# Optimization experiments

Hardware: AMD Instinct MI355X
Metric: run time of the kernel (lower is better)

## Reference

```python
import jax, jax.numpy as jnp
import numpy as np
from jax import lax

B, L, R = 128, 256, 36
D_TXT, D_IMG, D_SOC = 768, 2048, 10
EPS = 0.05 ** 2        # geomloss blur=0.05, p=2 -> epsilon = blur^p
N_ITERS = 20           # fixed log-domain Sinkhorn iterations
GAMMA = 0.01


def _pcost(x, y):
    # x: [B,n,d], y: [B,m,d] -> C_ij = ||x_i - y_j||^2 / 2 (geomloss p=2 cost)
    xx = jnp.sum(x * x, -1)[:, :, None]
    yy = jnp.sum(y * y, -1)[:, None, :]
    xy = jnp.einsum('bnd,bmd->bnm', x, y)
    return 0.5 * (xx + yy - 2.0 * xy)


def _sinkhorn_cost(C, loga, logb, eps, n_iters):
    # Log-domain Sinkhorn; masked points carry loga/logb = -inf (zero weight).
    f = jnp.zeros(loga.shape, C.dtype)
    g = jnp.zeros(logb.shape, C.dtype)

    def body(fg, _):
        f, g = fg
        g = -eps * jax.nn.logsumexp(loga[:, :, None] + (f[:, :, None] - C) / eps, axis=1)
        f = -eps * jax.nn.logsumexp(logb[:, None, :] + (g[:, None, :] - C) / eps, axis=2)
        return (f, g), None

    (f, g), _ = lax.scan(body, (f, g), None, length=n_iters)
    a = jnp.exp(loga)  # exp(-inf) = 0 for masked entries
    b = jnp.exp(logb)
    return jnp.sum(a * f, -1) + jnp.sum(b * g, -1)  # <a,f> + <b,g>


def _forward(txt_global, txt_region, img_global, img_region, social, attn_mask,
             W_stat, b_stat, W_gt, b_gt, W_gi, b_gi, W_rt, b_rt, W_ri, b_ri,
             W_m1, b_m1, W_m2, b_m2):
    relu = jax.nn.relu
    soc = relu(social @ W_stat + b_stat)                            # [B,100]
    tg = relu(jnp.concatenate([txt_global, soc], axis=1) @ W_gt + b_gt)  # [B,200]
    ig = relu(img_global @ W_gi + b_gi)                              # [B,200]
    h = relu((tg + ig) @ W_m1 + b_m1)
    mix_pred = h @ W_m2 + b_m2                                       # [B,2]

    tr = relu(txt_region @ W_rt + b_rt)                              # [B,L,50]
    ir = relu(img_region @ W_ri + b_ri)                              # [B,R,50]

    Bn, _, _ = tr.shape
    Rn = ir.shape[1]
    mask = attn_mask > 0
    n_words = jnp.sum(attn_mask, axis=-1).astype(tr.dtype)          # [B]
    loga = jnp.where(mask, -jnp.log(n_words)[:, None], -jnp.inf)    # uniform over valid tokens
    logb = jnp.full((Bn, Rn), -jnp.log(float(Rn)), tr.dtype)        # uniform over regions

    # Debiased Sinkhorn divergence (geomloss SamplesLoss default debias=True):
    Sxy = _sinkhorn_cost(_pcost(tr, ir), loga, logb, EPS, N_ITERS)
    Sxx = _sinkhorn_cost(_pcost(tr, tr), loga, loga, EPS, N_ITERS)
    Syy = _sinkhorn_cost(_pcost(ir, ir), logb, logb, EPS, N_ITERS)
    w_dis = Sxy - 0.5 * (Sxx + Syy)                                  # [B]

    w_pred = jnp.stack([1.0 - GAMMA * w_dis, GAMMA * w_dis], axis=1)  # [B,2]
    logit = jax.nn.softmax(jnp.maximum(mix_pred, w_pred), axis=1)
    return logit


def setup_inputs() -> dict:
    key = jax.random.key(0)
    ks = jax.random.split(key, 24)
    init = lambda k, s: (jax.random.normal(k, s) * 0.02).astype(jnp.float32)
    lengths = jax.random.randint(ks[0], (B,), 16, L + 1)             # ragged lengths
    attn_mask = (jnp.arange(L)[None, :] < lengths[:, None]).astype(jnp.int32)
    return {
        'txt_global': jax.random.normal(ks[1], (B, D_TXT), jnp.float32),
        'txt_region': jax.random.normal(ks[2], (B, L, D_TXT), jnp.float32),
        'img_global': jax.random.normal(ks[3], (B, D_IMG), jnp.float32),
        'img_region': jax.random.normal(ks[4], (B, R, D_IMG), jnp.float32),
        'social': jax.random.normal(ks[5], (B, D_SOC), jnp.float32),
        'attn_mask': attn_mask,
        'W_stat': init(ks[6], (D_SOC, 100)), 'b_stat': jnp.zeros((100,), jnp.float32),
        'W_gt': init(ks[7], (868, 200)), 'b_gt': jnp.zeros((200,), jnp.float32),
        'W_gi': init(ks[8], (D_IMG, 200)), 'b_gi': jnp.zeros((200,), jnp.float32),
        'W_rt': init(ks[9], (D_TXT, 50)), 'b_rt': jnp.zeros((50,), jnp.float32),
        'W_ri': init(ks[10], (D_IMG, 50)), 'b_ri': jnp.zeros((50,), jnp.float32),
        'W_m1': init(ks[11], (200, 100)), 'b_m1': jnp.zeros((100,), jnp.float32),
        'W_m2': init(ks[12], (100, 2)), 'b_m2': jnp.zeros((2,), jnp.float32),
    }


def reference(txt_global, txt_region, img_global, img_region, social, attn_mask,
              W_stat, b_stat, W_gt, b_gt, W_gi, b_gi, W_rt, b_rt, W_ri, b_ri,
              W_m1, b_m1, W_m2, b_m2):
    return _forward(txt_global, txt_region, img_global, img_region, social, attn_mask,
                    W_stat, b_stat, W_gt, b_gt, W_gi, b_gi, W_rt, b_rt, W_ri, b_ri,
                    W_m1, b_m1, W_m2, b_m2)
```

## Files before the change

### kernel.cpp

```cpp
#include <hip/hip_runtime.h>

typedef float        f32x4 __attribute__((ext_vector_type(4)));
typedef short        s16x8 __attribute__((ext_vector_type(8)));
typedef unsigned int u32x4 __attribute__((ext_vector_type(4)));

#define EPS_LN2      0.0017328679513998632f
#define INV_EPS_LN2  577.0780163555852f
#define LOG2_36      5.169925001442312f

__device__ __forceinline__ short f2bf(float x) {
  unsigned int u; __builtin_memcpy(&u, &x, 4);
  u = (u + 0x7FFFu + ((u >> 16) & 1u)) >> 16;
  return (short)u;
}

__device__ __forceinline__ unsigned short f2h(float x) {
  return __builtin_bit_cast(unsigned short, (_Float16)x);
}
__device__ __forceinline__ float h2f(unsigned short h) {
  return (float)__builtin_bit_cast(_Float16, h);
}

#define GLOAD16(g, l) __builtin_amdgcn_global_load_lds( \
    (const __attribute__((address_space(1))) void*)(g), \
    (__attribute__((address_space(3))) void*)(l), 16, 0, 0)

__global__ __launch_bounds__(256) void k_prep(
    const float* __restrict__ W_rt, const float* __restrict__ W_ri,
    short* __restrict__ frt, short* __restrict__ fri,
    const float* __restrict__ txt, const float* __restrict__ img,
    const float* __restrict__ social,
    const float* __restrict__ W_stat, const float* __restrict__ b_stat,
    const float* __restrict__ W_gt, const float* __restrict__ W_gi,
    float* __restrict__ pre) {
  __shared__ float sA[32][128];
  int bid = blockIdx.x;
  if (bid < 88) {
    int slot = bid * 256 + threadIdx.x;
    const float* W; short* dst; int f;
    if (slot < 6144) { W = W_rt; dst = frt; f = slot; }
    else             { W = W_ri; dst = fri; f = slot - 6144; }
    int k32 = f >> 8, rem = f & 255, ct = rem >> 6, l = rem & 63;
    int col = ct * 16 + (l & 15);
    int k0  = k32 * 32 + (l >> 4) * 8;
    s16x8 p;
#pragma unroll
    for (int c = 0; c < 8; ++c) {
      float v = (col < 50) ? W[(k0 + c) * 50 + col] : 0.f;
      p[c] = f2bf(v);
    }
    *(s16x8*)(dst + (long)f * 8) = p;
    return;
  }
  int gb = bid - 88;
  int job = gb >> 4, rb = (gb >> 2) & 3, cb = gb & 3;
  int t = threadIdx.x, r0 = rb * 32;
  const float* W; int k0, klen;
  if (job < 6)       { k0 = job * 128;       klen = 128; W = W_gt; }
  else if (job == 6) { k0 = 0;               klen = 100; W = W_gt + 768 * 200; }
  else               { k0 = (job - 7) * 128; klen = 128; W = W_gi; }
  if (job == 6) {
    for (int idx = t; idx < 4096; idx += 256) {
      int r = idx >> 7, k = idx & 127;
      float v = 0.f;
      if (k < 100) {
        v = b_stat[k];
#pragma unroll
        for (int u = 0; u < 10; ++u) v += social[(r0 + r) * 10 + u] * W_stat[u * 100 + k];
        v = fmaxf(v, 0.f);
      }
      sA[r][k] = v;
    }
  } else {
    const float* A = (job < 6) ? txt : img;
    int K_A = (job < 6) ? 768 : 2048;
    for (int idx = t; idx < 4096; idx += 256) {
      int r = idx >> 7, k = idx & 127;
      sA[r][k] = A[(r0 + r) * K_A + k0 + k];
    }
  }
  __syncthreads();
  int c = cb * 64 + (t & 63), rg = t >> 6;
  if (c < 200) {
    float acc[8];
#pragma unroll
    for (int i = 0; i < 8; ++i) acc[i] = 0.f;
    for (int k4 = 0; k4 < klen; k4 += 4) {
      float w0 = W[(k0 + k4    ) * 200 + c];
      float w1 = W[(k0 + k4 + 1) * 200 + c];
      float w2 = W[(k0 + k4 + 2) * 200 + c];
      float w3 = W[(k0 + k4 + 3) * 200 + c];
#pragma unroll
      for (int i = 0; i < 8; ++i) {
        f32x4 a = *(const f32x4*)&sA[rg * 8 + i][k4];
        acc[i] += a[0]*w0 + a[1]*w1 + a[2]*w2 + a[3]*w3;
      }
    }
    float* dst = pre + (long)job * 25600;
#pragma unroll
    for (int i = 0; i < 8; ++i)
      dst[(r0 + rg * 8 + i) * 200 + c] = acc[i];
  }
}

template<int K32>
__device__ __forceinline__ void proj_body(const float* __restrict__ A,
                                          const short* __restrict__ Bf,
                                          const float* __restrict__ bias,
                                          float* __restrict__ out, int bid,
                                          char* smem) {
  constexpr int KH = K32 / 2;
  int wave = threadIdx.x >> 6, lane = threadIdx.x & 63;
  int rg = wave >> 1, ks = wave & 1;
  int rl = lane & 15, q = lane >> 4, r7 = rl & 7;
  int row0 = bid * 32 + rg * 16;
  const int K = K32 * 32;
  char* wbuf = smem + wave * 18432;

  int ra = lane >> 3, pa = lane & 7;
  int fsw = (pa ^ ra) * 4;
  const float* asrc0 = A + (long)(row0 + ra)     * K + ks * (KH * 32) + fsw;
  const float* asrc1 = A + (long)(row0 + 8 + ra) * K + ks * (KH * 32) + fsw;
  const short* bsrc  = Bf + (long)ks * (KH * 2048) + lane * 8;

#define PSTAGE(KK, ST) { \
    char* ad = wbuf + (ST) * 6144; \
    GLOAD16(asrc0 + (KK) * 32, ad); \
    GLOAD16(asrc1 + (KK) * 32, ad + 1024); \
    char* bd = ad + 2048; \
    const short* bs = bsrc + (KK) * 2048; \
    GLOAD16(bs,        bd); \
    GLOAD16(bs + 512,  bd + 1024); \
    GLOAD16(bs + 1024, bd + 2048); \
    GLOAD16(bs + 1536, bd + 3072); \
  }

  f32x4 acc[4];
#pragma unroll
  for (int ct = 0; ct < 4; ++ct) acc[ct] = (f32x4){0.f, 0.f, 0.f, 0.f};

  PSTAGE(0, 0);
  PSTAGE(1, 1);
#pragma unroll
  for (int k = 0; k < KH; ++k) {
    if (k + 2 < KH) {
      PSTAGE(k + 2, (k + 2) % 3);
      asm volatile("s_waitcnt vmcnt(12)" ::: "memory");
    } else if (k + 2 == KH) {
      asm volatile("s_waitcnt vmcnt(6)" ::: "memory");
    } else {
      asm volatile("s_waitcnt vmcnt(0)" ::: "memory");
    }
    __builtin_amdgcn_sched_barrier(0);
    const char* ab = wbuf + (k % 3) * 6144;
    f32x4 a0 = *(const f32x4*)(ab + rl * 128 + (((q * 2)     ^ r7) << 4));
    f32x4 a1 = *(const f32x4*)(ab + rl * 128 + (((q * 2 + 1) ^ r7) << 4));
    const char* bb = ab + 2048;
    s16x8 af;
    af[0]=f2bf(a0[0]); af[1]=f2bf(a0[1]); af[2]=f2bf(a0[2]); af[3]=f2bf(a0[3]);
    af[4]=f2bf(a1[0]); af[5]=f2bf(a1[1]); af[6]=f2bf(a1[2]); af[7]=f2bf(a1[3]);
#pragma unroll
    for (int ct = 0; ct < 4; ++ct) {
      s16x8 bfr = *(const s16x8*)(bb + ct * 1024 + lane * 16);
      acc[ct] = __builtin_amdgcn_mfma_f32_16x16x32_bf16(af, bfr, acc[ct], 0, 0, 0);
    }
  }
#undef PSTAGE

  if (ks == 1) {
#pragma unroll
    for (int ct = 0; ct < 4; ++ct)
      *(f32x4*)(wbuf + ct * 1024 + lane * 16) = acc[ct];
  }
  __syncthreads();
  if (ks == 0) {
    const char* pb = smem + (wave + 1) * 18432;
#pragma unroll
    for (int ct = 0; ct < 4; ++ct) {
      f32x4 o = *(const f32x4*)(pb + ct * 1024 + lane * 16);
      int col = ct * 16 + rl;
      float bv = (col < 50) ? bias[col] : 0.f;
#pragma unroll
      for (int r = 0; r < 4; ++r) {
        int grow = row0 + q * 4 + r;
        float v = fmaxf(acc[ct][r] + o[r] + bv, 0.f);
        out[(long)grow * 64 + col] = (col < 50) ? v : 0.f;
      }
    }
  }
}

__device__ __forceinline__ void mix_body(
    int r, const float* __restrict__ pre,
    const float* __restrict__ b_gt, const float* __restrict__ b_gi,
    const float* __restrict__ W_m1, const float* __restrict__ b_m1,
    const float* __restrict__ W_m2, const float* __restrict__ b_m2,
    float* __restrict__ mix, float* smem) {
  float* sm = smem;
  float* sh = smem + 200;
  int t = threadIdx.x;
  if (t < 200) {
    float s1 = b_gt[t], s2 = b_gi[t];
#pragma unroll
    for (int j = 0; j < 7; ++j)  s1 += pre[(long)j * 25600 + r * 200 + t];
#pragma unroll
    for (int j = 7; j < 23; ++j) s2 += pre[(long)j * 25600 + r * 200 + t];
    sm[t] = fmaxf(s1, 0.f) + fmaxf(s2, 0.f);
  }
  __syncthreads();
  if (t < 100) {
    float a = b_m1[t];
#pragma unroll 4
    for (int k = 0; k < 200; ++k) a += sm[k] * W_m1[k * 100 + t];
    sh[t] = fmaxf(a, 0.f);
  }
  __syncthreads();
  if (t < 2) {
    float a = b_m2[t];
    for (int k = 0; k < 100; ++k) a += sh[k] * W_m2[k * 2 + t];
    mix[r * 2 + t] = a;
  }
}

__global__ __launch_bounds__(256)
void k_pm(
    const float* __restrict__ txt_region, const short* __restrict__ frt,
    const float* __restrict__ b_rt, float* __restrict__ tr,
    const float* __restrict__ img_region, const short* __restrict__ fri,
    const float* __restrict__ b_ri, float* __restrict__ ir,
    const float* __restrict__ pre,
    const float* __restrict__ b_gt, const float* __restrict__ b_gi,
    const float* __restrict__ W_m1, const float* __restrict__ b_m1,
    const float* __restrict__ W_m2, const float* __restrict__ b_m2,
    float* __restrict__ mix) {
  __shared__ __align__(16) char smem[73728];
  int bid = blockIdx.x;
  if (bid < 144)       proj_body<64>(img_region, fri, b_ri, ir, bid, smem);
  else if (bid < 1168) proj_body<24>(txt_region, frt, b_rt, tr, bid - 144, smem);
  else                 mix_body(bid - 1168, pre, b_gt, b_gi, W_m1, b_m1, W_m2, b_m2, mix, (float*)smem);
}

__global__ __launch_bounds__(256) void k_sxx(
    const float* __restrict__ tr, const int* __restrict__ amask,
    float* __restrict__ norms_g, float* __restrict__ Sxx) {
  __shared__ __align__(16) char smem[163840];
  char*  CT = smem;
  short* Xf = (short*)(smem + 131072);
  float*     sF   = (float*)(smem + 131072);
  float*     sG   = (float*)(smem + 132096);
  _Float16*  sA0  = (_Float16*)(smem + 133120);
  _Float16*  sA1  = (_Float16*)(smem + 133632);
  int b = blockIdx.x, tid = threadIdx.x;
  int lane = tid & 63, wv = tid >> 6;
  int q = lane >> 4, rl = lane & 15;

  int c = 0;
#pragma unroll
  for (int i = 0; i < 4; ++i) c += amask[b * 256 + i * 64 + lane];
#pragma unroll
  for (int o = 1; o < 64; o <<= 1) c += __shfl_xor(c, o);
  int n = __builtin_amdgcn_readfirstlane(c);

  const float* Xg = tr + (long)b * 256 * 64;
  for (int slot = tid; slot < 2048; slot += 256) {
    int t = slot >> 7, k32 = (slot >> 6) & 1, l = slot & 63;
    int row = t * 16 + (l & 15), k0 = k32 * 32 + (l >> 4) * 8;
    const float* src = Xg + row * 64 + k0;
    f32x4 a0 = *(const f32x4*)src, a1 = *(const f32x4*)(src + 4);
    s16x8 p;
    p[0]=f2bf(a0[0]); p[1]=f2bf(a0[1]); p[2]=f2bf(a0[2]); p[3]=f2bf(a0[3]);
    p[4]=f2bf(a1[0]); p[5]=f2bf(a1[1]); p[6]=f2bf(a1[2]); p[7]=f2bf(a1[3]);
    *(s16x8*)(Xf + slot * 8) = p;
  }
  __syncthreads();

  float* ng = norms_g + b * 256;
#pragma unroll
  for (int si = 0; si < 4; ++si) {
    int st = wv * 4 + si;
    s16x8 a0 = *(const s16x8*)(Xf + ((st * 2 + 0) * 64 + lane) * 8);
    s16x8 a1 = *(const s16x8*)(Xf + ((st * 2 + 1) * 64 + lane) * 8);
    f32x4 d = (f32x4){0.f, 0.f, 0.f, 0.f};
    d = __builtin_amdgcn_mfma_f32_16x16x32_bf16(a0, a0, d, 0, 0, 0);
    d = __builtin_amdgcn_mfma_f32_16x16x32_bf16(a1, a1, d, 0, 0, 0);
#pragma unroll
    for (int r = 0; r < 4; ++r)
      if (rl == q * 4 + r) ng[st * 16 + q * 4 + r] = d[r];
  }
  __syncthreads();

  float nj[16];
#pragma unroll
  for (int ct = 0; ct < 16; ++ct) nj[ct] = ng[ct * 16 + rl];

#pragma unroll
  for (int si = 0; si < 4; ++si) {
    int st = wv * 4 + si;
    int i0w = st * 16 + q * 4;
    float ni0 = ng[i0w], ni1 = ng[i0w + 1], ni2 = ng[i0w + 2], ni3 = ng[i0w + 3];
    s16x8 a0 = *(const s16x8*)(Xf + ((st * 2 + 0) * 64 + lane) * 8);
    s16x8 a1 = *(const s16x8*)(Xf + ((st * 2 + 1) * 64 + lane) * 8);
    f32x4 acc[16];
#pragma unroll
    for (int ct = 0; ct < 16; ++ct) acc[ct] = (f32x4){0.f, 0.f, 0.f, 0.f};
#pragma unroll
    for (int ct = 0; ct < 16; ++ct) {
      s16x8 b0 = *(const s16x8*)(Xf + ((ct * 2 + 0) * 64 + lane) * 8);
      s16x8 b1 = *(const s16x8*)(Xf + ((ct * 2 + 1) * 64 + lane) * 8);
      acc[ct] = __builtin_amdgcn_mfma_f32_16x16x32_bf16(a0, b0, acc[ct], 0, 0, 0);
      acc[ct] = __builtin_amdgcn_mfma_f32_16x16x32_bf16(a1, b1, acc[ct], 0, 0, 0);
    }
#pragma unroll
    for (int ct = 0; ct < 16; ++ct) {
      int j = ct * 16 + rl;
      float njv = nj[ct];
      float v0 = (acc[ct][0] - 0.5f * (ni0 + njv)) * INV_EPS_LN2;
      float v1 = (acc[ct][1] - 0.5f * (ni1 + njv)) * INV_EPS_LN2;
      float v2 = (acc[ct][2] - 0.5f * (ni2 + njv)) * INV_EPS_LN2;
      float v3 = (acc[ct][3] - 0.5f * (ni3 + njv)) * INV_EPS_LN2;
      char* p = CT + (((j << 9) + (i0w << 1)) ^ ((j & 7) << 4));
      *(unsigned*)(p)     = (unsigned)f2h(v0) | ((unsigned)f2h(v1) << 16);
      *(unsigned*)(p + 4) = (unsigned)f2h(v2) | ((unsigned)f2h(v3) << 16);
    }
  }
  __syncthreads();

  float log2n = log2f((float)n);
  sF[tid] = 0.f; sG[tid] = 0.f;
  sA0[tid] = (tid < n) ? (_Float16)(-log2n) : (_Float16)(-65504.f);
  sA1[tid] = (_Float16)(-65504.f);
  __syncthreads();

  int j = tid;
  unsigned base = (unsigned)(j << 9);
  unsigned sw   = (unsigned)((j & 7) << 4);
  int ns = (n + 7) >> 3;
  for (int h = 0; h < 40; ++h) {
    const unsigned* ah2 = (const unsigned*)((h & 1) ? sA1 : sA0);
    _Float16* aout = (h & 1) ? sA0 : sA1;
    if (j < n) {
      unsigned mm = 0xFBFFFBFFu;
      for (int s = 0; s < ns; ++s) {
        u32x4 v = *(const u32x4*)(CT + ((base + (unsigned)(s << 4)) ^ sw));
        unsigned a0 = ah2[s * 4 + 0], a1 = ah2[s * 4 + 1];
        unsigned a2 = ah2[s * 4 + 2], a3 = ah2[s * 4 + 3];
        unsigned t0, t1, t2, t3;
        asm("v_pk_add_f16 %0, %1, %2" : "=v"(t0) : "v"(v[0]), "v"(a0));
        asm("v_pk_add_f16 %0, %1, %2" : "=v"(t1) : "v"(v[1]), "v"(a1));
        asm("v_pk_add_f16 %0, %1, %2" : "=v"(t2) : "v"(v[2]), "v"(a2));
        asm("v_pk_add_f16 %0, %1, %2" : "=v"(t3) : "v"(v[3]), "v"(a3));
        asm("v_pk_max_f16 %0, %0, %1" : "+v"(mm) : "v"(t0));
        asm("v_pk_max_f16 %0, %0, %1" : "+v"(mm) : "v"(t1));
        asm("v_pk_max_f16 %0, %0, %1" : "+v"(mm) : "v"(t2));
        asm("v_pk_max_f16 %0, %0, %1" : "+v"(mm) : "v"(t3));
      }
      float m = fmaxf(h2f((unsigned short)(mm & 0xFFFFu)),
                      h2f((unsigned short)(mm >> 16)));
      ((h & 1) ? sF : sG)[j] = -EPS_LN2 * m;
      aout[j] = (_Float16)(-log2n - m);
    }
    __syncthreads();
  }
  if (tid < 64) {
    float a = 0.f;
    for (int i = tid; i < n; i += 64) a += sF[i] + sG[i];
#pragma unroll
    for (int o = 1; o < 64; o <<= 1) a += __shfl_xor(a, o);
    if (tid == 0) Sxx[b] = a / n;
  }
}

#define SK_SMEM 50736

__global__ __launch_bounds__(1024) void k_sxy(
    const float* __restrict__ tr, const float* __restrict__ ir,
    const int* __restrict__ amask,
    float* __restrict__ Sxy, float* __restrict__ Syy) {
  __shared__ __align__(16) char smem[SK_SMEM];
  int role = blockIdx.x >> 7;
  int b    = blockIdx.x & 127;
  int tid  = threadIdx.x;

  if (role == 0) {
    float* Ys  = (float*)smem;
    float* Cs  = (float*)(smem + 9216);
    float* nx  = (float*)(smem + 47104);
    float* ny  = (float*)(smem + 48128);
    float* sA  = (float*)(smem + 48288);
    float* sB  = (float*)(smem + 49376);
    float* sF  = (float*)(smem + 49536);
    float* sG  = (float*)(smem + 50560);
    int*   nsh = (int*)  (smem + 50720);
    if (tid < 64) {
      int c = 0;
      for (int i = tid; i < 256; i += 64) c += amask[b * 256 + i];
#pragma unroll
      for (int o = 1; o < 64; o <<= 1) c += __shfl_xor(c, o);
      if (tid == 0) *nsh = c;
    }
    const float* Xg = tr + (long)b * 256 * 64;
    const float* Yg = ir + (long)b * 36 * 64;
    for (int idx = tid; idx < 576; idx += 1024) {
      int row = idx >> 4, q4 = idx & 15;
      *(f32x4*)(Ys + row * 64 + q4 * 4) = *(const f32x4*)(Yg + row * 64 + q4 * 4);
    }
    __syncthreads();
    int n = *nsh;
    if (tid < 256) {
      float a = 0.f;
#pragma unroll
      for (int q4 = 0; q4 < 13; ++q4) {
        f32x4 v = *(const f32x4*)(Xg + tid * 64 + q4 * 4);
        a += v[0]*v[0] + v[1]*v[1] + v[2]*v[2] + v[3]*v[3];
      }
      nx[tid] = a;
    } else if (tid < 292) {
      int jj = tid - 256; float a = 0.f;
#pragma unroll
      for (int q4 = 0; q4 < 13; ++q4) {
        f32x4 v = *(const f32x4*)(Ys + jj * 64 + q4 * 4);
        a += v[0]*v[0] + v[1]*v[1] + v[2]*v[2] + v[3]*v[3];
      }
      ny[jj] = a;
    }
    __syncthreads();
    if (tid < 1008) {
      int ii = tid / 36, jj = tid - ii * 36;
      f32x4 yr[13];
#pragma unroll
      for (int q4 = 0; q4 < 13; ++q4) yr[q4] = *(const f32x4*)(Ys + jj * 64 + q4 * 4);
      float nyj = ny[jj];
      for (int i = ii; i < 256; i += 28) {
        float d = 0.f;
#pragma unroll
        for (int q4 = 0; q4 < 13; ++q4) {
          f32x4 xv = *(const f32x4*)(Xg + i * 64 + q4 * 4);
          d += xv[0]*yr[q4][0] + xv[1]*yr[q4][1] + xv[2]*yr[q4][2] + xv[3]*yr[q4][3];
        }
        Cs[i * 37 + jj] = (d - 0.5f * (nx[i] + nyj)) * INV_EPS_LN2;
      }
    }
    __syncthreads();
    int jg = tid >> 4, kg = tid & 15;
    float Cg[16];
    if (jg < 36) {
#pragma unroll
      for (int t = 0; t < 16; ++t) Cg[t] = Cs[(kg * 16 + t) * 37 + jg];
    }
    int fi = tid >> 2, kf = tid & 3;
    float Cf[9];
#pragma unroll
    for (int t = 0; t < 9; ++t) {
      int jj2 = kf * 9 + t;
      Cf[t] = (jj2 < 36) ? Cs[fi * 37 + jj2] : 0.f;
    }
    float log2n = log2f((float)n);
    if (tid < 256) { sF[tid] = 0.f; sA[tid + (tid >> 4)] = -log2n; }
    __syncthreads();
    const float* agp = sA + kg * 17;
    int gend = n - kg * 16; if (gend > 16) gend = 16;
    for (int it = 0; it < 20; ++it) {
      float gm = -1e30f;
      if (jg < 36) {
#pragma unroll
        for (int t = 0; t < 16; ++t)
          if (t < gend) gm = fmaxf(gm, agp[t] + Cg[t]);
        gm = fmaxf(gm, __shfl_xor(gm, 1)); gm = fmaxf(gm, __shfl_xor(gm, 2));
        gm = fmaxf(gm, __shfl_xor(gm, 4)); gm = fmaxf(gm, __shfl_xor(gm, 8));
      }
      __syncthreads();
      if (jg < 36 && kg == 0) {
        sG[jg] = -EPS_LN2 * gm;
        sB[jg] = -LOG2_36 - gm;
      }
      __syncthreads();
      float fm = -1e30f;
#pragma unroll
      for (int t = 0; t < 9; ++t) {
        int jj2 = kf * 9 + t;
        if (jj2 < 36) fm = fmaxf(fm, sB[jj2] + Cf[t]);
      }
      fm = fmaxf(fm, __shfl_xor(fm, 1)); fm = fmaxf(fm, __shfl_xor(fm, 2));
      __syncthreads();
      if (kf == 0 && fi < n) {
        sF[fi] = -EPS_LN2 * fm;
        sA[fi + (fi >> 4)] = -log2n - fm;
      }
      __syncthreads();
    }
    if (tid < 64) {
      float a = 0.f;
      for (int i = tid; i < n; i += 64) a += sF[i];
      float g = (tid < 36) ? sG[tid] : 0.f;
#pragma unroll
      for (int o = 1; o < 64; o <<= 1) { a += __shfl_xor(a, o); g += __shfl_xor(g, o); }
      if (tid == 0) Sxy[b] = a / n + g / 36.f;
    }
  } else {
    float* Ys = (float*)smem;
    float* Cs = (float*)(smem + 9216);
    float* ny = (float*)(smem + 48128);
    float* sA = (float*)(smem + 48288);
    float* sF = (float*)(smem + 49536);
    float* sG = (float*)(smem + 50560);
    const float* Yg = ir + (long)b * 36 * 64;
    for (int idx = tid; idx < 576; idx += 1024) {
      int row = idx >> 4, q4 = idx & 15;
      *(f32x4*)(Ys + row * 64 + q4 * 4) = *(const f32x4*)(Yg + row * 64 + q4 * 4);
    }
    __syncthreads();
    if (tid < 36) {
      float a = 0.f;
#pragma unroll
      for (int q4 = 0; q4 < 13; ++q4) {
        f32x4 v = *(const f32x4*)(Ys + tid * 64 + q4 * 4);
        a += v[0]*v[0] + v[1]*v[1] + v[2]*v[2] + v[3]*v[3];
      }
      ny[tid] = a;
    }
    __syncthreads();
    if (tid < 1008) {
      int ii = tid / 36, jj = tid - ii * 36;
      f32x4 yr[13];
#pragma unroll
      for (int q4 = 0; q4 < 13; ++q4) yr[q4] = *(const f32x4*)(Ys + jj * 64 + q4 * 4);
      float nyj = ny[jj];
      for (int i = ii; i < 36; i += 28) {
        float d = 0.f;
#pragma unroll
        for (int q4 = 0; q4 < 13; ++q4) {
          f32x4 xv = *(const f32x4*)(Ys + i * 64 + q4 * 4);
          d += xv[0]*yr[q4][0] + xv[1]*yr[q4][1] + xv[2]*yr[q4][2] + xv[3]*yr[q4][3];
        }
        Cs[i * 37 + jj] = (d - 0.5f * (ny[i] + nyj)) * INV_EPS_LN2;
      }
    }
    __syncthreads();
    int j = tid >> 2, kk = tid & 3;
    float Creg[9];
    if (j < 36) {
#pragma unroll
      for (int t = 0; t < 9; ++t) {
        int i2 = kk * 9 + t;
        Creg[t] = (i2 < 36) ? Cs[i2 * 37 + j] : 0.f;
      }
    }
    if (tid < 36) { sF[tid] = 0.f; sA[tid] = -LOG2_36; }
    __syncthreads();
    for (int h = 0; h < 40; ++h) {
      float m = -1e30f;
      if (j < 36) {
#pragma unroll
        for (int t = 0; t < 9; ++t) {
          int i2 = kk * 9 + t;
          if (i2 < 36) m = fmaxf(m, sA[i2] + Creg[t]);
        }
        m = fmaxf(m, __shfl_xor(m, 1)); m = fmaxf(m, __shfl_xor(m, 2));
      }
      __syncthreads();
      if (j < 36 && kk == 0) {
        ((h & 1) ? sF : sG)[j] = -EPS_LN2 * m;
        sA[j] = -LOG2_36 - m;
      }
      __syncthreads();
    }
    if (tid < 64) {
      float a = (tid < 36) ? sF[tid] + sG[tid] : 0.f;
#pragma unroll
      for (int o = 1; o < 64; o <<= 1) a += __shfl_xor(a, o);
      if (tid == 0) Syy[b] = a / 36.f;
    }
  }
}

__global__ void k_final(const float* __restrict__ mix, const float* __restrict__ sxy,
                        const float* __restrict__ sxx, const float* __restrict__ syy,
                        float* __restrict__ out) {
  int b = blockIdx.x * 64 + threadIdx.x;
  if (b < 128) {
    float w  = sxy[b] - 0.5f * (sxx[b] + syy[b]);
    float x0 = fmaxf(mix[b * 2 + 0], 1.0f - 0.01f * w);
    float x1 = fmaxf(mix[b * 2 + 1], 0.01f * w);
    float mx = fmaxf(x0, x1);
    float e0 = expf(x0 - mx), e1 = expf(x1 - mx);
    float inv = 1.f / (e0 + e1);
    out[b * 2 + 0] = e0 * inv;
    out[b * 2 + 1] = e1 * inv;
  }
}

extern "C" void kernel_launch(void* const* d_in, const int* in_sizes, int n_in,
                              void* d_out, int out_size, void* d_ws, size_t ws_size,
                              hipStream_t stream) {
  const float* txt_global = (const float*)d_in[0];
  const float* txt_region = (const float*)d_in[1];
  const float* img_global = (const float*)d_in[2];
  const float* img_region = (const float*)d_in[3];
  const float* social     = (const float*)d_in[4];
  const int*   attn_mask  = (const int*)  d_in[5];
  const float* W_stat = (const float*)d_in[6];  const float* b_stat = (const float*)d_in[7];
  const float* W_gt   = (const float*)d_in[8];  const float* b_gt   = (const float*)d_in[9];
  const float* W_gi   = (const float*)d_in[10]; const float* b_gi   = (const float*)d_in[11];
  const float* W_rt   = (const float*)d_in[12]; const float* b_rt   = (const float*)d_in[13];
  const float* W_ri   = (const float*)d_in[14]; const float* b_ri   = (const float*)d_in[15];
  const float* W_m1   = (const float*)d_in[16]; const float* b_m1   = (const float*)d_in[17];
  const float* W_m2   = (const float*)d_in[18]; const float* b_m2   = (const float*)d_in[19];

  float* ws = (float*)d_ws;
  float* ws_mix = ws;
  float* ws_sxy = ws + 256;
  float* ws_sxx = ws + 384;
  float* ws_syy = ws + 512;
  short* ws_frt = (short*)(ws + 1024);
  short* ws_fri = (short*)(ws + 25600);
  float* ws_tr  = ws + 131072;
  float* ws_ir  = ws + 2228224;
  float* ws_pre = ws + 2523136;
  float* ws_nrm = ws + 3111936;

  k_prep<<<456, 256, 0, stream>>>(W_rt, W_ri, ws_frt, ws_fri,
                                  txt_global, img_global, social,
                                  W_stat, b_stat, W_gt, W_gi, ws_pre);
  k_pm<<<1296, 256, 0, stream>>>(txt_region, ws_frt, b_rt, ws_tr,
                                 img_region, ws_fri, b_ri, ws_ir,
                                 ws_pre, b_gt, b_gi,
                                 W_m1, b_m1, W_m2, b_m2, ws_mix);
  k_sxx<<<128, 256, 0, stream>>>(ws_tr, attn_mask, ws_nrm, ws_sxx);
  k_sxy<<<256, 1024, 0, stream>>>(ws_tr, ws_ir, attn_mask, ws_sxy, ws_syy);
  k_final<<<2, 64, 0, stream>>>(ws_mix, ws_sxy, ws_sxx, ws_syy, (float*)d_out);
}
```

Measured before the change: 399.6 us.

## Split Sinkhorn self-term reduction across 512 threads and load projection operands into registers

k_sxx now runs 512 threads per batch. Each half of the threads covers half of the source range in the 40 log-domain half-iterations, and the two partial maxima are combined through LDS with an extra barrier per iteration. The norms now stay in shared memory instead of a global workspace. The projection body drops LDS staging through global_load_lds and issues triple-buffered global_load_dwordx4 directly into registers, which shrinks k_pm's shared memory from 72 KB to 8 KB. The risks are higher register pressure in the projection path and the extra synchronization per Sinkhorn step.

```diff
diff --git a/kernel.cpp b/kernel.cpp
--- a/kernel.cpp
+++ b/kernel.cpp
@@ -20,10 +20,6 @@
 __device__ __forceinline__ float h2f(unsigned short h) {
   return (float)__builtin_bit_cast(_Float16, h);
 }
-
-#define GLOAD16(g, l) __builtin_amdgcn_global_load_lds( \
-    (const __attribute__((address_space(1))) void*)(g), \
-    (__attribute__((address_space(3))) void*)(l), 16, 0, 0)
 
 __global__ __launch_bounds__(256) void k_prep(
     const float* __restrict__ W_rt, const float* __restrict__ W_ri,
@@ -108,43 +104,38 @@
                                           const short* __restrict__ Bf,
                                           const float* __restrict__ bias,
                                           float* __restrict__ out, int bid,
-                                          char* smem) {
+                                          float* __restrict__ red) {
   constexpr int KH = K32 / 2;
   int wave = threadIdx.x >> 6, lane = threadIdx.x & 63;
   int rg = wave >> 1, ks = wave & 1;
-  int rl = lane & 15, q = lane >> 4, r7 = rl & 7;
+  int rl = lane & 15, q = lane >> 4;
   int row0 = bid * 32 + rg * 16;
   const int K = K32 * 32;
-  char* wbuf = smem + wave * 18432;
-
-  int ra = lane >> 3, pa = lane & 7;
-  int fsw = (pa ^ ra) * 4;
-  const float* asrc0 = A + (long)(row0 + ra)     * K + ks * (KH * 32) + fsw;
-  const float* asrc1 = A + (long)(row0 + 8 + ra) * K + ks * (KH * 32) + fsw;
-  const short* bsrc  = Bf + (long)ks * (KH * 2048) + lane * 8;
-
-#define PSTAGE(KK, ST) { \
-    char* ad = wbuf + (ST) * 6144; \
-    GLOAD16(asrc0 + (KK) * 32, ad); \
-    GLOAD16(asrc1 + (KK) * 32, ad + 1024); \
-    char* bd = ad + 2048; \
-    const short* bs = bsrc + (KK) * 2048; \
-    GLOAD16(bs,        bd); \
-    GLOAD16(bs + 512,  bd + 1024); \
-    GLOAD16(bs + 1024, bd + 2048); \
-    GLOAD16(bs + 1536, bd + 3072); \
-  }
+  const float* ar = A + (long)(row0 + rl) * K + ks * (KH * 32) + q * 8;
+  const s16x8* bp = (const s16x8*)Bf + ks * (KH * 256) + lane;
+
+  f32x4 pa0[3], pa1[3];
+  s16x8 pb0[3], pb1[3], pb2[3], pb3[3];
+
+#define GLF(D, P) asm volatile("global_load_dwordx4 %0, %1, off" \
+                               : "=&v"(D) : "v"(P) : "memory")
+#define ISSUE(KK, S) { \
+    const float* ap_ = ar + (KK) * 32; \
+    GLF(pa0[S], ap_); GLF(pa1[S], ap_ + 4); \
+    const s16x8* bp_ = bp + (KK) * 256; \
+    GLF(pb0[S], bp_); GLF(pb1[S], bp_ + 64); \
+    GLF(pb2[S], bp_ + 128); GLF(pb3[S], bp_ + 192); }
 
   f32x4 acc[4];
 #pragma unroll
   for (int ct = 0; ct < 4; ++ct) acc[ct] = (f32x4){0.f, 0.f, 0.f, 0.f};
 
-  PSTAGE(0, 0);
-  PSTAGE(1, 1);
+  ISSUE(0, 0);
+  ISSUE(1, 1);
 #pragma unroll
   for (int k = 0; k < KH; ++k) {
     if (k + 2 < KH) {
-      PSTAGE(k + 2, (k + 2) % 3);
+      ISSUE(k + 2, (k + 2) % 3);
       asm volatile("s_waitcnt vmcnt(12)" ::: "memory");
     } else if (k + 2 == KH) {
       asm volatile("s_waitcnt vmcnt(6)" ::: "memory");
@@ -152,32 +143,31 @@
       asm volatile("s_waitcnt vmcnt(0)" ::: "memory");
     }
     __builtin_amdgcn_sched_barrier(0);
-    const char* ab = wbuf + (k % 3) * 6144;
-    f32x4 a0 = *(const f32x4*)(ab + rl * 128 + (((q * 2)     ^ r7) << 4));
-    f32x4 a1 = *(const f32x4*)(ab + rl * 128 + (((q * 2 + 1) ^ r7) << 4));
-    const char* bb = ab + 2048;
+    int s = k % 3;
     s16x8 af;
-    af[0]=f2bf(a0[0]); af[1]=f2bf(a0[1]); af[2]=f2bf(a0[2]); af[3]=f2bf(a0[3]);
-    af[4]=f2bf(a1[0]); af[5]=f2bf(a1[1]); af[6]=f2bf(a1[2]); af[7]=f2bf(a1[3]);
+    af[0]=f2bf(pa0[s][0]); af[1]=f2bf(pa0[s][1]);
+    af[2]=f2bf(pa0[s][2]); af[3]=f2bf(pa0[s][3]);
+    af[4]=f2bf(pa1[s][0]); af[5]=f2bf(pa1[s][1]);
+    af[6]=f2bf(pa1[s][2]); af[7]=f2bf(pa1[s][3]);
+    acc[0] = __builtin_amdgcn_mfma_f32_16x16x32_bf16(af, pb0[s], acc[0], 0, 0, 0);
+    acc[1] = __builtin_amdgcn_mfma_f32_16x16x32_bf16(af, pb1[s], acc[1], 0, 0, 0);
+    acc[2] = __builtin_amdgcn_mfma_f32_16x16x32_bf16(af, pb2[s], acc[2], 0, 0, 0);
+    acc[3] = __builtin_amdgcn_mfma_f32_16x16x32_bf16(af, pb3[s], acc[3], 0, 0, 0);
+  }
+#undef ISSUE
+#undef GLF
+
+  float* rb = red + rg * 1024;
+  if (ks == 1) {
+#pragma unroll
+    for (int ct = 0; ct < 4; ++ct)
+      *(f32x4*)(rb + lane * 16 + ct * 4) = acc[ct];
+  }
+  __syncthreads();
+  if (ks == 0) {
 #pragma unroll
     for (int ct = 0; ct < 4; ++ct) {
-      s16x8 bfr = *(const s16x8*)(bb + ct * 1024 + lane * 16);
-      acc[ct] = __builtin_amdgcn_mfma_f32_16x16x32_bf16(af, bfr, acc[ct], 0, 0, 0);
-    }
-  }
-#undef PSTAGE
-
-  if (ks == 1) {
-#pragma unroll
-    for (int ct = 0; ct < 4; ++ct)
-      *(f32x4*)(wbuf + ct * 1024 + lane * 16) = acc[ct];
-  }
-  __syncthreads();
-  if (ks == 0) {
-    const char* pb = smem + (wave + 1) * 18432;
-#pragma unroll
-    for (int ct = 0; ct < 4; ++ct) {
-      f32x4 o = *(const f32x4*)(pb + ct * 1024 + lane * 16);
+      f32x4 o = *(const f32x4*)(rb + lane * 16 + ct * 4);
       int col = ct * 16 + rl;
       float bv = (col < 50) ? bias[col] : 0.f;
 #pragma unroll
@@ -233,23 +223,24 @@
     const float* __restrict__ W_m1, const float* __restrict__ b_m1,
     const float* __restrict__ W_m2, const float* __restrict__ b_m2,
     float* __restrict__ mix) {
-  __shared__ __align__(16) char smem[73728];
+  __shared__ __align__(16) float red[2048];
   int bid = blockIdx.x;
-  if (bid < 144)       proj_body<64>(img_region, fri, b_ri, ir, bid, smem);
-  else if (bid < 1168) proj_body<24>(txt_region, frt, b_rt, tr, bid - 144, smem);
-  else                 mix_body(bid - 1168, pre, b_gt, b_gi, W_m1, b_m1, W_m2, b_m2, mix, (float*)smem);
-}
-
-__global__ __launch_bounds__(256) void k_sxx(
+  if (bid < 144)       proj_body<64>(img_region, fri, b_ri, ir, bid, red);
+  else if (bid < 1168) proj_body<24>(txt_region, frt, b_rt, tr, bid - 144, red);
+  else                 mix_body(bid - 1168, pre, b_gt, b_gi, W_m1, b_m1, W_m2, b_m2, mix, red);
+}
+
+__global__ __launch_bounds__(512) void k_sxx(
     const float* __restrict__ tr, const int* __restrict__ amask,
-    float* __restrict__ norms_g, float* __restrict__ Sxx) {
+    float* __restrict__ Sxx) {
   __shared__ __align__(16) char smem[163840];
-  char*  CT = smem;
-  short* Xf = (short*)(smem + 131072);
-  float*     sF   = (float*)(smem + 131072);
-  float*     sG   = (float*)(smem + 132096);
-  _Float16*  sA0  = (_Float16*)(smem + 133120);
-  _Float16*  sA1  = (_Float16*)(smem + 133632);
+  char*  CT    = smem;
+  float* norms = (float*)smem;
+  short* Xf    = (short*)(smem + 131072);
+  float*     sPm = (float*)(smem + 131072);
+  float*     sF  = (float*)(smem + 133120);
+  float*     sG  = (float*)(smem + 134144);
+  _Float16*  sAh = (_Float16*)(smem + 135168);
   int b = blockIdx.x, tid = threadIdx.x;
   int lane = tid & 63, wv = tid >> 6;
   int q = lane >> 4, rl = lane & 15;
@@ -262,7 +253,7 @@
   int n = __builtin_amdgcn_readfirstlane(c);
 
   const float* Xg = tr + (long)b * 256 * 64;
-  for (int slot = tid; slot < 2048; slot += 256) {
+  for (int slot = tid; slot < 2048; slot += 512) {
     int t = slot >> 7, k32 = (slot >> 6) & 1, l = slot & 63;
     int row = t * 16 + (l & 15), k0 = k32 * 32 + (l >> 4) * 8;
     const float* src = Xg + row * 64 + k0;
@@ -274,10 +265,9 @@
   }
   __syncthreads();
 
-  float* ng = norms_g + b * 256;
-#pragma unroll
-  for (int si = 0; si < 4; ++si) {
-    int st = wv * 4 + si;
+#pragma unroll
+  for (int si = 0; si < 2; ++si) {
+    int st = wv * 2 + si;
     s16x8 a0 = *(const s16x8*)(Xf + ((st * 2 + 0) * 64 + lane) * 8);
     s16x8 a1 = *(const s16x8*)(Xf + ((st * 2 + 1) * 64 + lane) * 8);
     f32x4 d = (f32x4){0.f, 0.f, 0.f, 0.f};
@@ -285,19 +275,26 @@
     d = __builtin_amdgcn_mfma_f32_16x16x32_bf16(a1, a1, d, 0, 0, 0);
 #pragma unroll
     for (int r = 0; r < 4; ++r)
-      if (rl == q * 4 + r) ng[st * 16 + q * 4 + r] = d[r];
+      if (rl == q * 4 + r) norms[st * 16 + q * 4 + r] = d[r];
   }
   __syncthreads();
 
   float nj[16];
 #pragma unroll
-  for (int ct = 0; ct < 16; ++ct) nj[ct] = ng[ct * 16 + rl];
-
-#pragma unroll
-  for (int si = 0; si < 4; ++si) {
-    int st = wv * 4 + si;
+  for (int ct = 0; ct < 16; ++ct) nj[ct] = norms[ct * 16 + rl];
+  float ni[2][4];
+#pragma unroll
+  for (int si = 0; si < 2; ++si) {
+    int base = (wv * 2 + si) * 16 + q * 4;
+#pragma unroll
+    for (int r = 0; r < 4; ++r) ni[si][r] = norms[base + r];
+  }
+  __syncthreads();
+
+#pragma unroll
+  for (int si = 0; si < 2; ++si) {
+    int st = wv * 2 + si;
     int i0w = st * 16 + q * 4;
-    float ni0 = ng[i0w], ni1 = ng[i0w + 1], ni2 = ng[i0w + 2], ni3 = ng[i0w + 3];
     s16x8 a0 = *(const s16x8*)(Xf + ((st * 2 + 0) * 64 + lane) * 8);
     s16x8 a1 = *(const s16x8*)(Xf + ((st * 2 + 1) * 64 + lane) * 8);
     f32x4 acc[16];
@@ -314,10 +311,10 @@
     for (int ct = 0; ct < 16; ++ct) {
       int j = ct * 16 + rl;
       float njv = nj[ct];
-      float v0 = (acc[ct][0] - 0.5f * (ni0 + njv)) * INV_EPS_LN2;
-      float v1 = (acc[ct][1] - 0.5f * (ni1 + njv)) * INV_EPS_LN2;
-      float v2 = (acc[ct][2] - 0.5f * (ni2 + njv)) * INV_EPS_LN2;
-      float v3 = (acc[ct][3] - 0.5f * (ni3 + njv)) * INV_EPS_LN2;
+      float v0 = (acc[ct][0] - 0.5f * (ni[si][0] + njv)) * INV_EPS_LN2;
+      float v1 = (acc[ct][1] - 0.5f * (ni[si][1] + njv)) * INV_EPS_LN2;
+      float v2 = (acc[ct][2] - 0.5f * (ni[si][2] + njv)) * INV_EPS_LN2;
+      float v3 = (acc[ct][3] - 0.5f * (ni[si][3] + njv)) * INV_EPS_LN2;
       char* p = CT + (((j << 9) + (i0w << 1)) ^ ((j & 7) << 4));
       *(unsigned*)(p)     = (unsigned)f2h(v0) | ((unsigned)f2h(v1) << 16);
       *(unsigned*)(p + 4) = (unsigned)f2h(v2) | ((unsigned)f2h(v3) << 16);
@@ -326,21 +323,23 @@
   __syncthreads();
 
   float log2n = log2f((float)n);
-  sF[tid] = 0.f; sG[tid] = 0.f;
-  sA0[tid] = (tid < n) ? (_Float16)(-log2n) : (_Float16)(-65504.f);
-  sA1[tid] = (_Float16)(-65504.f);
-  __syncthreads();
-
-  int j = tid;
+  if (tid < 256) {
+    sF[tid] = 0.f; sG[tid] = 0.f;
+    sAh[tid] = (tid < n) ? (_Float16)(-log2n) : (_Float16)(-65504.f);
+  }
+  __syncthreads();
+
+  int kk = tid >> 8, j = tid & 255;
   unsigned base = (unsigned)(j << 9);
   unsigned sw   = (unsigned)((j & 7) << 4);
-  int ns = (n + 7) >> 3;
+  int smaxAll = (n + 7) >> 3;
+  int smin = kk * 16;
+  int smax = smaxAll < (kk + 1) * 16 ? smaxAll : (kk + 1) * 16;
+  const unsigned* ah2 = (const unsigned*)sAh;
   for (int h = 0; h < 40; ++h) {
-    const unsigned* ah2 = (const unsigned*)((h & 1) ? sA1 : sA0);
-    _Float16* aout = (h & 1) ? sA0 : sA1;
+    unsigned mm = 0xFBFFFBFFu;
     if (j < n) {
-      unsigned mm = 0xFBFFFBFFu;
-      for (int s = 0; s < ns; ++s) {
+      for (int s = smin; s < smax; ++s) {
         u32x4 v = *(const u32x4*)(CT + ((base + (unsigned)(s << 4)) ^ sw));
         unsigned a0 = ah2[s * 4 + 0], a1 = ah2[s * 4 + 1];
         unsigned a2 = ah2[s * 4 + 2], a3 = ah2[s * 4 + 3];
@@ -354,10 +353,16 @@
         asm("v_pk_max_f16 %0, %0, %1" : "+v"(mm) : "v"(t2));
         asm("v_pk_max_f16 %0, %0, %1" : "+v"(mm) : "v"(t3));
       }
-      float m = fmaxf(h2f((unsigned short)(mm & 0xFFFFu)),
-                      h2f((unsigned short)(mm >> 16)));
-      ((h & 1) ? sF : sG)[j] = -EPS_LN2 * m;
-      aout[j] = (_Float16)(-log2n - m);
+    }
+    sPm[kk * 256 + j] = fmaxf(h2f((unsigned short)(mm & 0xFFFFu)),
+                              h2f((unsigned short)(mm >> 16)));
+    __syncthreads();
+    if (tid < 256) {
+      float m2 = fmaxf(sPm[tid], sPm[256 + tid]);
+      if (tid < n) {
+        ((h & 1) ? sF : sG)[tid] = -EPS_LN2 * m2;
+        sAh[tid] = (_Float16)(-log2n - m2);
+      }
     }
     __syncthreads();
   }
@@ -616,7 +621,6 @@
   float* ws_tr  = ws + 131072;
   float* ws_ir  = ws + 2228224;
   float* ws_pre = ws + 2523136;
-  float* ws_nrm = ws + 3111936;
 
   k_prep<<<456, 256, 0, stream>>>(W_rt, W_ri, ws_frt, ws_fri,
                                   txt_global, img_global, social,
@@ -625,7 +629,7 @@
                                  img_region, ws_fri, b_ri, ws_ir,
                                  ws_pre, b_gt, b_gi,
                                  W_m1, b_m1, W_m2, b_m2, ws_mix);
-  k_sxx<<<128, 256, 0, stream>>>(ws_tr, attn_mask, ws_nrm, ws_sxx);
+  k_sxx<<<128, 512, 0, stream>>>(ws_tr, attn_mask, ws_sxx);
   k_sxy<<<256, 1024, 0, stream>>>(ws_tr, ws_ir, attn_mask, ws_sxy, ws_syy);
   k_final<<<2, 64, 0, stream>>>(ws_mix, ws_sxy, ws_sxx, ws_syy, (float*)d_out);
 }
```

Measured after the change: 366.5 us. 1.09x faster.
